# Performance work log

Hardware: AMD Instinct MI355X
Metric: run time of the kernel (lower is better)

The kernel has to match this reference:

```python
import jax, jax.numpy as jnp
import numpy as np

LEAK = 0.95
EPS = 1e-4
THRESH = 1.0


def spike_fn(x):
    # forward of SurrogateBPFunction: heaviside(x > 0)
    return (x > 0).astype(x.dtype)


def setup_inputs() -> dict:
    key = jax.random.key(0)
    k1, k2, k3 = jax.random.split(key, 3)
    T, B, D_in, H, C = 20, 512, 4096, 1024, 100
    z = jax.random.normal(k1, (T, B, D_in), dtype=jnp.float32)
    # xavier_uniform with gain=2: bound = 2 * sqrt(6/(fan_in+fan_out))
    b1 = 2.0 * np.sqrt(6.0 / (D_in + H))
    W1 = jax.random.uniform(k2, (H, D_in), dtype=jnp.float32, minval=-b1, maxval=b1)
    b2 = 2.0 * np.sqrt(6.0 / (H + C))
    W2 = jax.random.uniform(k3, (C, H), dtype=jnp.float32, minval=-b2, maxval=b2)
    bn_gamma = jnp.ones((T, H), dtype=jnp.float32)
    return {"z": z, "W1": W1, "bn_gamma": bn_gamma, "W2": W2}


def reference(z, W1, bn_gamma, W2):
    T = z.shape[0]
    B = z.shape[1]
    H = W1.shape[0]
    C = W2.shape[0]

    def step(carry, xs):
        mem1, mem2 = carry
        inp_t, gamma = xs  # inp_t: [B, D_in], gamma: [H]
        h = jnp.einsum('bd,hd->bh', inp_t, W1)  # fc1, no bias
        # BatchNorm1d (training-mode batch stats, affine weight, no bias)
        mean = h.mean(axis=0)
        var = h.var(axis=0)  # biased variance, matches torch BN
        h = gamma * (h - mean) * jax.lax.rsqrt(var + EPS)
        mem1 = LEAK * mem1 + h
        mem_thr = mem1 / THRESH - 1.0
        out = spike_fn(mem_thr)
        rst = jnp.where(mem_thr > 0, THRESH, 0.0).astype(mem1.dtype)
        mem1 = mem1 - rst
        mem2 = mem2 + jnp.einsum('bh,ch->bc', out, W2)
        return (mem1, mem2), None

    mem1_0 = jnp.zeros((B, H), dtype=z.dtype)
    mem2_0 = jnp.zeros((B, C), dtype=z.dtype)
    (mem1, mem2), _ = jax.lax.scan(step, (mem1_0, mem2_0), (z, bn_gamma))
    return mem2 / T
```

## Files before the change

### kernel.cpp

```cpp
#include <hip/hip_runtime.h>
#include <hip/hip_bf16.h>
#include <stdint.h>

typedef _Float16 half8 __attribute__((ext_vector_type(8)));
typedef float f32x4 __attribute__((ext_vector_type(4)));
typedef float f32x16 __attribute__((ext_vector_type(16)));

#define T_STEPS 20
#define B_SZ 512
#define D_IN 4096
#define H_SZ 1024
#define C_SZ 100
#define M_TOT (T_STEPS * B_SZ)
#define BK 32
#define KITERS (D_IN / BK)
#define KHALF (KITERS / 2)
#define HPLANE ((int64_t)M_TOT * H_SZ)

__device__ __forceinline__ void gload16(const _Float16* g, _Float16* l) {
  __builtin_amdgcn_global_load_lds(
      (const __attribute__((address_space(1))) void*)g,
      (__attribute__((address_space(3))) void*)l, 16, 0, 0);
}

struct HL {
  half8 h;
  half8 l;
};
__device__ __forceinline__ HL split8(float4 a, float4 b) {
  HL r;
  auto p0 = __builtin_amdgcn_cvt_pkrtz(a.x, a.y);
  auto p1 = __builtin_amdgcn_cvt_pkrtz(a.z, a.w);
  auto p2 = __builtin_amdgcn_cvt_pkrtz(b.x, b.y);
  auto p3 = __builtin_amdgcn_cvt_pkrtz(b.z, b.w);
  r.h[0] = p0.x; r.h[1] = p0.y; r.h[2] = p1.x; r.h[3] = p1.y;
  r.h[4] = p2.x; r.h[5] = p2.y; r.h[6] = p3.x; r.h[7] = p3.y;
  auto q0 = __builtin_amdgcn_cvt_pkrtz(a.x - (float)p0.x, a.y - (float)p0.y);
  auto q1 = __builtin_amdgcn_cvt_pkrtz(a.z - (float)p1.x, a.w - (float)p1.y);
  auto q2 = __builtin_amdgcn_cvt_pkrtz(b.x - (float)p2.x, b.y - (float)p2.y);
  auto q3 = __builtin_amdgcn_cvt_pkrtz(b.z - (float)p3.x, b.w - (float)p3.y);
  r.l[0] = q0.x; r.l[1] = q0.y; r.l[2] = q1.x; r.l[3] = q1.y;
  r.l[4] = q2.x; r.l[5] = q2.y; r.l[6] = q3.x; r.l[7] = q3.y;
  return r;
}

__global__ __launch_bounds__(256) void k_prep_frag(
    const float* __restrict__ Z, _Float16* __restrict__ Azh,
    _Float16* __restrict__ Azl, const float* __restrict__ W1,
    _Float16* __restrict__ Wfh, _Float16* __restrict__ Wfl) {
  __shared__ float sL[32 * 256];

  const int cc = blockIdx.x;
  int rt = blockIdx.y >> 2;
  const int rb = blockIdx.y & 3;
  const float* src;
  _Float16 *dh, *dl;
  if (rt < 80) {
    src = Z; dh = Azh; dl = Azl;
  } else {
    rt -= 80; src = W1; dh = Wfh; dl = Wfl;
  }
  const int tid = threadIdx.x;
  const int lane64 = tid & 63;
  const int w4 = tid >> 6;

  const int row_base = rt * 128 + rb * 32;
  float4 v[8];
#pragma unroll
  for (int it = 0; it < 8; ++it) {
    const int row_local = it * 4 + w4;
    v[it] = *(const float4*)(src + (int64_t)(row_base + row_local) * D_IN +
                             cc * 256 + lane64 * 4);
  }
#pragma unroll
  for (int it = 0; it < 8; ++it) {
    const int row_local = it * 4 + w4;
    const int c = (lane64 * 4) ^ ((row_local & 7) << 2);
    *(float4*)&sL[row_local * 256 + c] = v[it];
  }
  __syncthreads();

  const int s = (tid >> 6) & 1;
  const int hi = (tid >> 5) & 1;
  const int l31 = tid & 31;
  const int q = s * 2 + hi;
  const int sw = (l31 & 7) << 2;
#pragma unroll
  for (int it2 = 0; it2 < 4; ++it2) {
    const int kil = it2 * 2 + (tid >> 7);
    const int c0 = kil * 32 + q * 8;
    float4 a = *(const float4*)&sL[l31 * 256 + (c0 ^ sw)];
    float4 b = *(const float4*)&sL[l31 * 256 + ((c0 + 4) ^ sw)];
    HL hl = split8(a, b);
    const int64_t d = ((int64_t)(rt * 128 + cc * 8 + kil)) * 4096 +
                      (rb * 128 + s * 64 + hi * 32 + l31) * 8;
    *(half8*)&dh[d] = hl.h;
    *(half8*)&dl[d] = hl.l;
  }
}

__global__ void k_prep_w2(const float* __restrict__ w2, _Float16* __restrict__ hi,
                          _Float16* __restrict__ lo) {
  int i = blockIdx.x * 256 + threadIdx.x;
  float v = (i < C_SZ * H_SZ) ? w2[i] : 0.0f;
  _Float16 h = (_Float16)v;
  hi[i] = h;
  lo[i] = (_Float16)(v - (float)h);
}

__global__ __launch_bounds__(256) void k_gemm1(
    const _Float16* __restrict__ Ahi, const _Float16* __restrict__ Alo,
    const _Float16* __restrict__ Whi, const _Float16* __restrict__ Wlo,
    float* __restrict__ Hpart) {
  __shared__ _Float16 sAh[4096];
  __shared__ _Float16 sAl[4096];
  __shared__ _Float16 sWh[4096];
  __shared__ _Float16 sWl[4096];

  const int tid = threadIdx.x;
  const int lane = tid & 63;
  const int w = tid >> 6;

  const int bid = blockIdx.x;
  const int xcd = bid & 7;
  const int q = bid >> 3;
  const int mtl = q >> 4;
  const int r = q & 15;
  const int nt = r >> 1;
  const int kh = r & 1;
  const int mt = xcd * 10 + mtl;

  const int ls = w * 512 + lane * 8;
  const _Float16* gAh = Ahi + (int64_t)mt * (128 * 4096) + ls;
  const _Float16* gAl = Alo + (int64_t)mt * (128 * 4096) + ls;
  const _Float16* gWh = Whi + (int64_t)nt * (128 * 4096) + ls;
  const _Float16* gWl = Wlo + (int64_t)nt * (128 * 4096) + ls;

  const int wm = (w >> 1) * 64;
  const int wn = (w & 1) * 64;
  const int ra = (wm >> 4) * 512 + lane * 8;
  const int rbb = (wn >> 4) * 512 + lane * 8;

  f32x16 acc[2][2] = {};

  const int k0 = kh * KHALF;
  for (int ki = k0; ki < k0 + KHALF; ++ki) {
    const int64_t so = (int64_t)ki * 4096;
    __syncthreads();
    gload16(gAh + so, &sAh[ls]);
    gload16(gAh + so + 2048, &sAh[ls + 2048]);
    gload16(gAl + so, &sAl[ls]);
    gload16(gAl + so + 2048, &sAl[ls + 2048]);
    gload16(gWh + so, &sWh[ls]);
    gload16(gWh + so + 2048, &sWh[ls + 2048]);
    gload16(gWl + so, &sWl[ls]);
    gload16(gWl + so + 2048, &sWl[ls + 2048]);
    __syncthreads();

    half8 ah[2][2], al[2][2], bh[2][2], bl[2][2];
#pragma unroll
    for (int i = 0; i < 2; ++i) {
#pragma unroll
      for (int s = 0; s < 2; ++s) {
        ah[i][s] = *(const half8*)&sAh[ra + (i * 2 + s) * 512];
        al[i][s] = *(const half8*)&sAl[ra + (i * 2 + s) * 512];
        bh[i][s] = *(const half8*)&sWh[rbb + (i * 2 + s) * 512];
        bl[i][s] = *(const half8*)&sWl[rbb + (i * 2 + s) * 512];
      }
    }
#pragma unroll
    for (int a = 0; a < 2; ++a) {
#pragma unroll
      for (int b = 0; b < 2; ++b) {
#pragma unroll
        for (int s = 0; s < 2; ++s) {
          acc[a][b] = __builtin_amdgcn_mfma_f32_32x32x16_f16(ah[a][s], bh[b][s], acc[a][b], 0, 0, 0);
          acc[a][b] = __builtin_amdgcn_mfma_f32_32x32x16_f16(ah[a][s], bl[b][s], acc[a][b], 0, 0, 0);
          acc[a][b] = __builtin_amdgcn_mfma_f32_32x32x16_f16(al[a][s], bh[b][s], acc[a][b], 0, 0, 0);
        }
      }
    }
  }

  float* Hb = Hpart + (int64_t)kh * HPLANE;
  const int64_t m0 = (int64_t)mt * 128;
  const int n0 = nt * 128;
  const int l31 = lane & 31;
  const int h2 = lane >> 5;
#pragma unroll
  for (int a = 0; a < 2; ++a) {
#pragma unroll
    for (int b = 0; b < 2; ++b) {
      float* dst = Hb + (m0 + wm + a * 32 + h2 * 4) * H_SZ + n0 + wn + b * 32 + l31;
#pragma unroll
      for (int r4 = 0; r4 < 4; ++r4) {
#pragma unroll
        for (int rr = 0; rr < 4; ++rr) {
          dst[(int64_t)(r4 * 8 + rr) * H_SZ] = acc[a][b][r4 * 4 + rr];
        }
      }
    }
  }
}

__global__ void k_stats(const float* __restrict__ Hpart, const float* __restrict__ gamma,
                        float* __restrict__ scale, float* __restrict__ shift) {
  const int t = blockIdx.y;
  const int tx = threadIdx.x & 63;
  const int ty = threadIdx.x >> 6;
  const int h = blockIdx.x * 64 + tx;
  const float* p0 = Hpart + ((int64_t)t * B_SZ + ty * 128) * H_SZ + h;
  const float* p1 = p0 + HPLANE;
  float s = 0.f, s2 = 0.f;
#pragma unroll 8
  for (int i = 0; i < 128; ++i) {
    float v = p0[(int64_t)i * H_SZ] + p1[(int64_t)i * H_SZ];
    s += v;
    s2 += v * v;
  }
  __shared__ float ss[4][64];
  __shared__ float sq[4][64];
  ss[ty][tx] = s;
  sq[ty][tx] = s2;
  __syncthreads();
  if (ty == 0) {
    float a = ss[0][tx] + ss[1][tx] + ss[2][tx] + ss[3][tx];
    float b = sq[0][tx] + sq[1][tx] + sq[2][tx] + sq[3][tx];
    const float mean = a * (1.0f / B_SZ);
    const float var = b * (1.0f / B_SZ) - mean * mean;
    const float rs = rsqrtf(var + 1e-4f);
    const float sc = gamma[t * H_SZ + h] * rs;
    scale[t * H_SZ + h] = sc;
    shift[t * H_SZ + h] = -mean * sc;
  }
}

__global__ void k_recur(const float* __restrict__ Hpart, const float* __restrict__ scale,
                        const float* __restrict__ shift, _Float16* __restrict__ S) {
  const int idx = blockIdx.x * 256 + threadIdx.x;
  const int b = idx >> 10;
  const int h = idx & 1023;
  float mem = 0.f;
  int cnt = 0;
#pragma unroll
  for (int t = 0; t < T_STEPS; ++t) {
    const int64_t i = ((int64_t)(t * B_SZ + b) << 10) + h;
    float v = Hpart[i] + Hpart[i + HPLANE];
    v = v * scale[(t << 10) + h] + shift[(t << 10) + h];
    mem = 0.95f * mem + v;
    if (mem - 1.0f > 0.0f) {
      ++cnt;
      mem -= 1.0f;
    }
  }
  S[idx] = (_Float16)cnt;
}

__global__ void k_gemm2(const _Float16* __restrict__ S, const _Float16* __restrict__ W2h,
                        const _Float16* __restrict__ W2l, float* __restrict__ out) {
  const int wid = threadIdx.x >> 6;
  const int lane = threadIdx.x & 63;
  const int m0 = blockIdx.y * 64 + wid * 16;
  const int n0 = blockIdx.x * 16;
  const int fr = lane & 15;
  const int quad = lane >> 4;

  const _Float16* sp = S + (int64_t)(m0 + fr) * H_SZ + quad * 8;
  const _Float16* wph = W2h + (int64_t)(n0 + fr) * H_SZ + quad * 8;
  const _Float16* wpl = W2l + (int64_t)(n0 + fr) * H_SZ + quad * 8;

  f32x4 acc = {0.f, 0.f, 0.f, 0.f};
#pragma unroll 4
  for (int k = 0; k < H_SZ; k += 32) {
    half8 a = *(const half8*)(sp + k);
    half8 bh = *(const half8*)(wph + k);
    half8 bl = *(const half8*)(wpl + k);
    acc = __builtin_amdgcn_mfma_f32_16x16x32_f16(a, bh, acc, 0, 0, 0);
    acc = __builtin_amdgcn_mfma_f32_16x16x32_f16(a, bl, acc, 0, 0, 0);
  }
  const int col = n0 + fr;
  if (col < C_SZ) {
#pragma unroll
    for (int r = 0; r < 4; ++r) {
      const int row = m0 + quad * 4 + r;
      out[row * C_SZ + col] = acc[r] * (1.0f / T_STEPS);
    }
  }
}

extern "C" void kernel_launch(void* const* d_in, const int* in_sizes, int n_in,
                              void* d_out, int out_size, void* d_ws, size_t ws_size,
                              hipStream_t stream) {
  const float* z = (const float*)d_in[0];
  const float* W1 = (const float*)d_in[1];
  const float* gamma = (const float*)d_in[2];
  const float* W2 = (const float*)d_in[3];
  float* out = (float*)d_out;

  char* ws = (char*)d_ws;
  size_t off = 0;
  auto alloc = [&](size_t bytes) -> void* {
    void* p = ws + off;
    off += (bytes + 255) & ~(size_t)255;
    return p;
  };
  _Float16* Azh = (_Float16*)alloc((size_t)M_TOT * D_IN * 2);
  _Float16* Azl = (_Float16*)alloc((size_t)M_TOT * D_IN * 2);
  _Float16* Wfh = (_Float16*)alloc((size_t)H_SZ * D_IN * 2);
  _Float16* Wfl = (_Float16*)alloc((size_t)H_SZ * D_IN * 2);
  float* Hpart = (float*)alloc((size_t)2 * M_TOT * H_SZ * 4);
  float* scale = (float*)alloc((size_t)T_STEPS * H_SZ * 4);
  float* shift = (float*)alloc((size_t)T_STEPS * H_SZ * 4);
  _Float16* S = (_Float16*)alloc((size_t)B_SZ * H_SZ * 2);
  _Float16* W2h = (_Float16*)alloc((size_t)112 * H_SZ * 2);
  _Float16* W2l = (_Float16*)alloc((size_t)112 * H_SZ * 2);

  dim3 gp(16, 352);
  k_prep_frag<<<gp, 256, 0, stream>>>(z, Azh, Azl, W1, Wfh, Wfl);
  k_prep_w2<<<(112 * H_SZ) / 256, 256, 0, stream>>>(W2, W2h, W2l);

  k_gemm1<<<1280, 256, 0, stream>>>(Azh, Azl, Wfh, Wfl, Hpart);

  dim3 gs(H_SZ / 64, T_STEPS);
  k_stats<<<gs, 256, 0, stream>>>(Hpart, gamma, scale, shift);

  k_recur<<<(B_SZ * H_SZ) / 256, 256, 0, stream>>>(Hpart, scale, shift, S);

  dim3 g2(7, 8);
  k_gemm2<<<g2, 256, 0, stream>>>(S, W2h, W2l, out);
}
```

Measured before the change: 541.9 us.

## Load GEMM1 fragments directly from global memory instead of staging through LDS

Removes the LDS staging buffers and the two block barriers per K-iteration in the fc1 GEMM. Each wave now reads its MFMA operand fragments straight from the pre-swizzled global hi/lo arrays, with the loop unrolled by two. This drops synchronisation and LDS traffic. In exchange, operands shared between waves are fetched from global or cache once per wave instead of once per block, which raises global load volume and exposes load latency.

```diff
diff --git a/kernel.cpp b/kernel.cpp
--- a/kernel.cpp
+++ b/kernel.cpp
@@ -16,12 +16,6 @@
 #define KITERS (D_IN / BK)
 #define KHALF (KITERS / 2)
 #define HPLANE ((int64_t)M_TOT * H_SZ)
-
-__device__ __forceinline__ void gload16(const _Float16* g, _Float16* l) {
-  __builtin_amdgcn_global_load_lds(
-      (const __attribute__((address_space(1))) void*)g,
-      (__attribute__((address_space(3))) void*)l, 16, 0, 0);
-}
 
 struct HL {
   half8 h;
@@ -112,11 +106,6 @@
     const _Float16* __restrict__ Ahi, const _Float16* __restrict__ Alo,
     const _Float16* __restrict__ Whi, const _Float16* __restrict__ Wlo,
     float* __restrict__ Hpart) {
-  __shared__ _Float16 sAh[4096];
-  __shared__ _Float16 sAl[4096];
-  __shared__ _Float16 sWh[4096];
-  __shared__ _Float16 sWl[4096];
-
   const int tid = threadIdx.x;
   const int lane = tid & 63;
   const int w = tid >> 6;
@@ -130,42 +119,30 @@
   const int kh = r & 1;
   const int mt = xcd * 10 + mtl;
 
-  const int ls = w * 512 + lane * 8;
-  const _Float16* gAh = Ahi + (int64_t)mt * (128 * 4096) + ls;
-  const _Float16* gAl = Alo + (int64_t)mt * (128 * 4096) + ls;
-  const _Float16* gWh = Whi + (int64_t)nt * (128 * 4096) + ls;
-  const _Float16* gWl = Wlo + (int64_t)nt * (128 * 4096) + ls;
-
   const int wm = (w >> 1) * 64;
   const int wn = (w & 1) * 64;
   const int ra = (wm >> 4) * 512 + lane * 8;
   const int rbb = (wn >> 4) * 512 + lane * 8;
 
+  const int k0 = kh * KHALF;
+  const _Float16* pAh = Ahi + (int64_t)mt * (128 * 4096) + (int64_t)k0 * 4096 + ra;
+  const _Float16* pAl = Alo + (int64_t)mt * (128 * 4096) + (int64_t)k0 * 4096 + ra;
+  const _Float16* pWh = Whi + (int64_t)nt * (128 * 4096) + (int64_t)k0 * 4096 + rbb;
+  const _Float16* pWl = Wlo + (int64_t)nt * (128 * 4096) + (int64_t)k0 * 4096 + rbb;
+
   f32x16 acc[2][2] = {};
 
-  const int k0 = kh * KHALF;
-  for (int ki = k0; ki < k0 + KHALF; ++ki) {
-    const int64_t so = (int64_t)ki * 4096;
-    __syncthreads();
-    gload16(gAh + so, &sAh[ls]);
-    gload16(gAh + so + 2048, &sAh[ls + 2048]);
-    gload16(gAl + so, &sAl[ls]);
-    gload16(gAl + so + 2048, &sAl[ls + 2048]);
-    gload16(gWh + so, &sWh[ls]);
-    gload16(gWh + so + 2048, &sWh[ls + 2048]);
-    gload16(gWl + so, &sWl[ls]);
-    gload16(gWl + so + 2048, &sWl[ls + 2048]);
-    __syncthreads();
-
+#pragma unroll 2
+  for (int ki = 0; ki < KHALF; ++ki) {
     half8 ah[2][2], al[2][2], bh[2][2], bl[2][2];
 #pragma unroll
     for (int i = 0; i < 2; ++i) {
 #pragma unroll
       for (int s = 0; s < 2; ++s) {
-        ah[i][s] = *(const half8*)&sAh[ra + (i * 2 + s) * 512];
-        al[i][s] = *(const half8*)&sAl[ra + (i * 2 + s) * 512];
-        bh[i][s] = *(const half8*)&sWh[rbb + (i * 2 + s) * 512];
-        bl[i][s] = *(const half8*)&sWl[rbb + (i * 2 + s) * 512];
+        ah[i][s] = *(const half8*)(pAh + (i * 2 + s) * 512);
+        al[i][s] = *(const half8*)(pAl + (i * 2 + s) * 512);
+        bh[i][s] = *(const half8*)(pWh + (i * 2 + s) * 512);
+        bl[i][s] = *(const half8*)(pWl + (i * 2 + s) * 512);
       }
     }
 #pragma unroll
@@ -180,6 +157,7 @@
         }
       }
     }
+    pAh += 4096; pAl += 4096; pWh += 4096; pWl += 4096;
   }
 
   float* Hb = Hpart + (int64_t)kh * HPLANE;
```

Result: slower. 642.9 us (+18.6%).
